# Kernel tuning notes

Hardware: AMD Instinct MI355X
Metric: run time of the kernel (lower is better)

## Reference

```python
import jax, jax.numpy as jnp
import numpy as np

B, N, D = 4, 512, 256  # batch, num_diseases, feature_dim == hidden_dim
H = 256                # hidden_dim
EPS = 1e-5

def _layernorm(x, g, b):
    m = jnp.mean(x, axis=-1, keepdims=True)
    v = jnp.mean((x - m) ** 2, axis=-1, keepdims=True)
    return (x - m) * jax.lax.rsqrt(v + EPS) * g + b

def setup_inputs() -> dict:
    key = jax.random.key(0)
    ks = jax.random.split(key, 16)
    s = 0.02
    return {
        "x": jax.random.normal(ks[0], (B, N, D), jnp.float32),
        "area_matrix": jax.random.uniform(ks[1], (B, N), jnp.float32),
        "co_occurrence": jax.random.uniform(ks[2], (N, N), jnp.float32),
        "Wq": jax.random.normal(ks[3], (H, D), jnp.float32) * s,
        "bq": jnp.zeros((H,), jnp.float32),
        "Wk": jax.random.normal(ks[4], (H, D), jnp.float32) * s,
        "bk": jnp.zeros((H,), jnp.float32),
        "Wv": jax.random.normal(ks[5], (H, D), jnp.float32) * s,
        "bv": jnp.zeros((H,), jnp.float32),
        "We1": jax.random.normal(ks[6], (H, 2), jnp.float32) * 0.5,
        "be1": jnp.zeros((H,), jnp.float32),
        "We2": jax.random.normal(ks[7], (1, H), jnp.float32) * s,
        "be2": jnp.zeros((1,), jnp.float32),
        "Wo": jax.random.normal(ks[8], (H, H), jnp.float32) * s,
        "bo": jnp.zeros((H,), jnp.float32),
        "g_ot": jnp.ones((H,), jnp.float32),
        "b_ot": jnp.zeros((H,), jnp.float32),
        "g1": jnp.ones((H,), jnp.float32),
        "b1": jnp.zeros((H,), jnp.float32),
        "g2": jnp.ones((H,), jnp.float32),
        "b2": jnp.zeros((H,), jnp.float32),
    }

def reference(x, area_matrix, co_occurrence, Wq, bq, Wk, bk, Wv, bv,
              We1, be1, We2, be2, Wo, bo, g_ot, b_ot, g1, b1, g2, b2):
    # projections: (B, N, H)
    q = jnp.einsum('bnd,hd->bnh', x, Wq) + bq
    k = jnp.einsum('bnd,hd->bnh', x, Wk) + bk
    v = jnp.einsum('bnd,hd->bnh', x, Wv) + bv
    attn_scores = jnp.einsum('bih,bjh->bij', q, k) / jnp.sqrt(jnp.float32(H))
    # edge inputs: (B, N, N, 2) = stack(broadcast area along last N, broadcast co-occ along batch)
    area = jnp.broadcast_to(area_matrix[:, :, None], (B, N, N))
    co = jnp.broadcast_to(co_occurrence[None], (B, N, N))
    edge_inputs = jnp.stack([area, co], axis=-1)
    h = jax.nn.relu(jnp.einsum('bije,he->bijh', edge_inputs, We1) + be1)
    edge_weights = jax.nn.sigmoid(jnp.einsum('bijh,oh->bijo', h, We2) + be2)[..., 0]
    attn_probs = jax.nn.softmax(attn_scores * edge_weights, axis=-1)  # dropout = identity (eval)
    out = jnp.einsum('bij,bjh->bih', attn_probs, v)
    out = _layernorm(out, g1, b1)
    out = jax.nn.relu(_layernorm(jnp.einsum('bnh,oh->bno', out, Wo) + bo, g_ot, b_ot))
    out = _layernorm(out + x, g2, b2)
    return out
```

## Files before the change

kernel.cpp:

```cpp
#include <hip/hip_runtime.h>

typedef unsigned short u16;
typedef unsigned int u32;

#define NB 4
#define NN 512
#define ND 256
#define NH 256
#define TI 4

typedef __attribute__((ext_vector_type(8))) short short8;
typedef __attribute__((ext_vector_type(4))) float f32x4;

__device__ __forceinline__ u16 bfq(float f) {
    u32 t; __builtin_memcpy(&t, &f, 4);
    u32 r = (t + 0x7FFFu + ((t >> 16) & 1u)) >> 16;
    return (u16)r;
}

__device__ __forceinline__ float waveReduceSum(float v) {
#pragma unroll
    for (int o = 32; o > 0; o >>= 1) v += __shfl_down(v, o);
    return v;
}

__device__ __forceinline__ void blockReduce8(float4& va, float4& vb, float4* red) {
#pragma unroll
    for (int o = 32; o > 0; o >>= 1) {
        va.x += __shfl_down(va.x, o); va.y += __shfl_down(va.y, o);
        va.z += __shfl_down(va.z, o); va.w += __shfl_down(va.w, o);
        vb.x += __shfl_down(vb.x, o); vb.y += __shfl_down(vb.y, o);
        vb.z += __shfl_down(vb.z, o); vb.w += __shfl_down(vb.w, o);
    }
    int wid = threadIdx.x >> 6;
    __syncthreads();
    if ((threadIdx.x & 63) == 0) { red[2 * wid] = va; red[2 * wid + 1] = vb; }
    __syncthreads();
    float4 ra = red[0], rb = red[1];
#pragma unroll
    for (int w = 1; w < 8; ++w) {
        float4 ua = red[2 * w], ub = red[2 * w + 1];
        ra.x += ua.x; ra.y += ua.y; ra.z += ua.z; ra.w += ua.w;
        rb.x += ub.x; rb.y += ub.y; rb.z += ub.z; rb.w += ub.w;
    }
    va = ra; vb = rb;
}

__global__ __launch_bounds__(256) void prep_kernel(
    const float* __restrict__ x, const float* __restrict__ Wq,
    const float* __restrict__ Wk, const float* __restrict__ Wv,
    const float* __restrict__ Wo,
    u16* __restrict__ xb, u16* __restrict__ wb)
{
    const int idx4 = (blockIdx.x * 256 + threadIdx.x) * 4;
    const float* src;
    u16* dst;
    int off;
    if (idx4 < 524288) { src = x; dst = xb; off = idx4; }
    else {
        int u = idx4 - 524288;
        int which = u >> 16; off = u & 65535;
        src = (which == 0) ? Wq : (which == 1) ? Wk : (which == 2) ? Wv : Wo;
        dst = wb + which * 65536;
    }
    float4 f = *(const float4*)(src + off);
    u32 lo = (u32)bfq(f.x) | ((u32)bfq(f.y) << 16);
    u32 hi = (u32)bfq(f.z) | ((u32)bfq(f.w) << 16);
    *(uint2*)(dst + off) = make_uint2(lo, hi);
}

__global__ __launch_bounds__(256) void qkv_mfma(
    const u16* __restrict__ xb, const u16* __restrict__ wb,
    const float* __restrict__ bq, const float* __restrict__ bk, const float* __restrict__ bv,
    u16* __restrict__ qb, u16* __restrict__ kb, u16* __restrict__ vt)
{
    const int lane = threadIdx.x & 63, wave = threadIdx.x >> 6;
    const int r0 = blockIdx.x * 64 + wave * 16;
    const int out0 = blockIdx.y * 16;
    const int which = blockIdx.y >> 4;
    const float* bia = (which == 0) ? bq : (which == 1) ? bk : bv;

    const int m = lane & 15, koff = (lane >> 4) * 8;
    const u16* Ap = xb + (size_t)(r0 + m) * 256 + koff;
    const u16* Bp = wb + which * 65536 + (size_t)((out0 & 255) + m) * 256 + koff;

    f32x4 acc = {0.f, 0.f, 0.f, 0.f};
#pragma unroll
    for (int ks = 0; ks < 8; ++ks) {
        short8 a  = *(const short8*)(Ap + ks * 32);
        short8 bb = *(const short8*)(Bp + ks * 32);
        acc = __builtin_amdgcn_mfma_f32_16x16x32_bf16(a, bb, acc, 0, 0, 0);
    }

    const int oc = (out0 + m) & 255;
    const float bias = bia[oc];
    const int rbase = r0 + (lane >> 4) * 4;
#pragma unroll
    for (int reg = 0; reg < 4; ++reg) {
        int R = rbase + reg;
        u16 val = bfq(acc[reg] + bias);
        if (which == 0)      qb[(size_t)R * 256 + oc] = val;
        else if (which == 1) kb[(size_t)R * 256 + oc] = val;
        else                 vt[((size_t)(R >> 9) * 256 + oc) * 512 + (R & 511)] = val;
    }
}

#define PSTR 520
#define YSTR 264
__global__ __launch_bounds__(512, 4) void fused_kernel(
    const float* __restrict__ x, const float* __restrict__ area, const float* __restrict__ co,
    const float* __restrict__ We1, const float* __restrict__ be1,
    const float* __restrict__ We2, const float* __restrict__ be2,
    const u16* __restrict__ wob, const float* __restrict__ bo,
    const float* __restrict__ g_ot, const float* __restrict__ b_ot,
    const float* __restrict__ g1, const float* __restrict__ b1,
    const float* __restrict__ g2, const float* __restrict__ b2,
    const u16* __restrict__ qb, const u16* __restrict__ kb,
    const u16* __restrict__ vt, float* __restrict__ out)
{
    const int tid = threadIdx.x;
    const int b = blockIdx.x >> 7;
    const int i0 = (blockIdx.x & 127) << 2;
    const int lane = tid & 63, w = tid >> 6;
    const int g = lane >> 4, c = lane & 15;
    const int hP = tid & 255, half = tid >> 8;

    __shared__ float histS[1024], histB[1024];
    __shared__ float pvbuf[1024];
    __shared__ u16 srow16[16 * PSTR];
    __shared__ u16 y16[16 * YSTR];
    __shared__ float4 red8b[16];
    __shared__ float sBaseS[4], sBaseB[4], redA[8], redB[8];

    const int m = lane & 15, koff = (lane >> 4) * 8;
    const u16* Ap    = qb + (size_t)(b * 512 + i0 + m) * 256 + koff;
    const u16* Kbase = kb + (size_t)(b * 512 + m) * 256 + koff;

    short8 afr[8];
#pragma unroll
    for (int ks = 0; ks < 8; ++ks) afr[ks] = *(const short8*)(Ap + ks * 32);
    short8 k0[4], k1[4];
#pragma unroll
    for (int ks = 0; ks < 4; ++ks)
        k0[ks] = *(const short8*)(Kbase + (size_t)(w * 4) * 16 * 256 + ks * 32);

    float cov[4];
#pragma unroll
    for (int t = 0; t < 4; ++t)
        cov[t] = co[(size_t)(i0 + g) * NN + (w * 4 + t) * 16 + c];

    float xv[TI];
#pragma unroll
    for (int ti = 0; ti < TI; ++ti)
        xv[ti] = x[(size_t)(b * NN + i0 + ti) * ND + hP];

    const float bov  = bo[hP];
    const float g1v  = g1[hP],  b1v  = b1[hP];
    const float gotv = g_ot[hP], botv = b_ot[hP];
    const float g2v  = g2[hP],  b2v  = b2[hP];
    const float be2f = be2[0];

    histS[tid] = 0.f; histS[tid + 512] = 0.f;
    histB[tid] = 0.f; histB[tid + 512] = 0.f;
    {
        u32* s32 = (u32*)srow16;
        for (int i = tid; i < 4160; i += 512) s32[i] = 0u;
        u32* y32 = (u32*)y16;
        for (int i = tid; i < 2112; i += 512) y32[i] = 0u;
    }
    __syncthreads();

    {
        const int s = tid >> 7, h0 = tid & 127;
        const float a = area[b * NN + i0 + s];
        float baS = 0.f, baB = 0.f;
#pragma unroll
        for (int k = 0; k < 2; ++k) {
            const int h = h0 + 128 * k;
            const float w10 = We1[2 * h], w11 = We1[2 * h + 1];
            const float w2v = We2[h], be1v = be1[h];
            const float al = fmaf(a, w10, be1v);
            const float sl = w11 * w2v, bb = al * w2v;
            if (w11 == 0.f) {
                if (al > 0.f) baB += bb;
            } else {
                float tt = -al / w11;
                if (w11 > 0.f) {
                    if (tt <= 0.f)      { baS += sl; baB += bb; }
                    else if (tt < 1.f) {
                        int u = (int)(tt * 256.f); u = u > 255 ? 255 : u;
                        atomicAdd(&histS[s * 256 + u], sl);
                        atomicAdd(&histB[s * 256 + u], bb);
                    }
                } else {
                    if (tt >= 1.f)      { baS += sl; baB += bb; }
                    else if (tt > 0.f) {
                        baS += sl; baB += bb;
                        int u = (int)(tt * 256.f); u = u > 255 ? 255 : u;
                        atomicAdd(&histS[s * 256 + u], -sl);
                        atomicAdd(&histB[s * 256 + u], -bb);
                    }
                }
            }
        }
        float rS = waveReduceSum(baS), rB = waveReduceSum(baB);
        if (lane == 0) { redA[w] = rS; redB[w] = rB; }
    }

    f32x4 sacc[4];
    {
#pragma unroll
        for (int t = 0; t < 4; ++t) {
            const u16* Bp = Kbase + (size_t)(w * 4 + t) * 16 * 256;
#pragma unroll
            for (int ks = 0; ks < 4; ++ks) k1[ks] = *(const short8*)(Bp + (ks + 4) * 32);
            f32x4 acc = {0.f, 0.f, 0.f, 0.f};
#pragma unroll
            for (int ks = 0; ks < 4; ++ks)
                acc = __builtin_amdgcn_mfma_f32_16x16x32_bf16(afr[ks], k0[ks], acc, 0, 0, 0);
            if (t < 3) {
                const u16* Bn = Kbase + (size_t)(w * 4 + t + 1) * 16 * 256;
#pragma unroll
                for (int ks = 0; ks < 4; ++ks) k0[ks] = *(const short8*)(Bn + ks * 32);
            }
#pragma unroll
            for (int ks = 0; ks < 4; ++ks)
                acc = __builtin_amdgcn_mfma_f32_16x16x32_bf16(afr[ks + 4], k1[ks], acc, 0, 0, 0);
            sacc[t] = acc;
        }
    }
    __syncthreads();
    if (tid < 4) {
        sBaseS[tid] = redA[2 * tid] + redA[2 * tid + 1];
        sBaseB[tid] = redB[2 * tid] + redB[2 * tid + 1];
    }

    {
        const int s = w & 3;
        float* hp = (w < 4) ? histS : histB;
        float b0 = hp[s * 256 + 4 * lane + 0];
        float b1 = hp[s * 256 + 4 * lane + 1];
        float b2 = hp[s * 256 + 4 * lane + 2];
        float b3 = hp[s * 256 + 4 * lane + 3];
        float p0 = b0, p1 = p0 + b1, p2 = p1 + b2, p3 = p2 + b3;
        float incl = p3;
#pragma unroll
        for (int off = 1; off < 64; off <<= 1) {
            float t = __shfl_up(incl, off);
            if (lane >= off) incl += t;
        }
        float excl = incl - p3;
        hp[s * 256 + 4 * lane + 0] = p0 + excl;
        hp[s * 256 + 4 * lane + 1] = p1 + excl;
        hp[s * 256 + 4 * lane + 2] = p2 + excl;
        hp[s * 256 + 4 * lane + 3] = p3 + excl;
    }
    __syncthreads();

    {
#pragma unroll
        for (int t = 0; t < 4; ++t) {
            const int j = (w * 4 + t) * 16 + c;
            float s0 = __shfl(sacc[t][0], c);
            float s1 = __shfl(sacc[t][1], c);
            float s2 = __shfl(sacc[t][2], c);
            float s3 = __shfl(sacc[t][3], c);
            float sv = (g == 0) ? s0 : (g == 1) ? s1 : (g == 2) ? s2 : s3;
            float cc = cov[t];
            int u = (int)(cc * 256.f); u = u > 255 ? 255 : u;
            float Sg = sBaseS[g] + histS[g * 256 + u];
            float Bg = sBaseB[g] + histB[g * 256 + u];
            float e = fmaf(cc, Sg, Bg) + be2f;
            float ew = 1.f / (1.f + __expf(-e));
            srow16[g * PSTR + j] = bfq(__expf(sv * 0.0625f * ew));
        }
    }
    __syncthreads();

    {
        const int t0 = 2 * w, t1 = 2 * w + 1;
        const u16* B0p = vt + ((size_t)(b * 256 + t0 * 16 + m)) * 512 + koff;
        const u16* B1p = vt + ((size_t)(b * 256 + t1 * 16 + m)) * 512 + koff;
        const u16* Arow = srow16 + m * PSTR + koff;
        f32x4 acc0 = {0.f, 0.f, 0.f, 0.f}, acc1 = {0.f, 0.f, 0.f, 0.f};
#pragma unroll
        for (int ks = 0; ks < 16; ++ks) {
            short8 a  = *(const short8*)(Arow + ks * 32);
            short8 b0 = *(const short8*)(B0p + ks * 32);
            short8 b1 = *(const short8*)(B1p + ks * 32);
            acc0 = __builtin_amdgcn_mfma_f32_16x16x32_bf16(a, b0, acc0, 0, 0, 0);
            acc1 = __builtin_amdgcn_mfma_f32_16x16x32_bf16(a, b1, acc1, 0, 0, 0);
        }
        if (lane < 16) {
#pragma unroll
            for (int reg = 0; reg < 4; ++reg) {
                pvbuf[reg * 256 + t0 * 16 + lane] = acc0[reg];
                pvbuf[reg * 256 + t1 * 16 + lane] = acc1[reg];
            }
        }
        __syncthreads();
    }

    float4 sa, sb;
    float accv[TI];
#pragma unroll
    for (int ti = 0; ti < TI; ++ti) {
        accv[ti] = (half == 0) ? pvbuf[ti * 256 + hP] : 0.f;
        ((float*)&sa)[ti] = accv[ti];
        ((float*)&sb)[ti] = accv[ti] * accv[ti];
    }
    blockReduce8(sa, sb, red8b);
    if (half == 0) {
#pragma unroll
        for (int ti = 0; ti < TI; ++ti) {
            float mean = ((const float*)&sa)[ti] * (1.f / 256.f);
            float var = fmaxf(((const float*)&sb)[ti] * (1.f / 256.f) - mean * mean, 0.f);
            y16[ti * YSTR + hP] = bfq((accv[ti] - mean) * rsqrtf(var + 1e-5f) * g1v + b1v);
        }
    }
    __syncthreads();

    {
        const int t0 = 2 * w, t1 = 2 * w + 1;
        const u16* B0p = wob + (size_t)(t0 * 16 + m) * 256 + koff;
        const u16* B1p = wob + (size_t)(t1 * 16 + m) * 256 + koff;
        const u16* Arow = y16 + m * YSTR + koff;
        f32x4 acc0 = {0.f, 0.f, 0.f, 0.f}, acc1 = {0.f, 0.f, 0.f, 0.f};
#pragma unroll
        for (int ks = 0; ks < 8; ++ks) {
            short8 a  = *(const short8*)(Arow + ks * 32);
            short8 b0 = *(const short8*)(B0p + ks * 32);
            short8 b1 = *(const short8*)(B1p + ks * 32);
            acc0 = __builtin_amdgcn_mfma_f32_16x16x32_bf16(a, b0, acc0, 0, 0, 0);
            acc1 = __builtin_amdgcn_mfma_f32_16x16x32_bf16(a, b1, acc1, 0, 0, 0);
        }
        if (lane < 16) {
#pragma unroll
            for (int reg = 0; reg < 4; ++reg) {
                pvbuf[reg * 256 + t0 * 16 + lane] = acc0[reg];
                pvbuf[reg * 256 + t1 * 16 + lane] = acc1[reg];
            }
        }
        __syncthreads();
    }

    float acc2[TI];
#pragma unroll
    for (int ti = 0; ti < TI; ++ti) {
        acc2[ti] = (half == 0) ? pvbuf[ti * 256 + hP] + bov : 0.f;
        ((float*)&sa)[ti] = acc2[ti];
        ((float*)&sb)[ti] = acc2[ti] * acc2[ti];
    }
    blockReduce8(sa, sb, red8b);
    float z[TI];
#pragma unroll
    for (int ti = 0; ti < TI; ++ti) {
        float mean = ((const float*)&sa)[ti] * (1.f / 256.f);
        float var = fmaxf(((const float*)&sb)[ti] * (1.f / 256.f) - mean * mean, 0.f);
        z[ti] = fmaxf((acc2[ti] - mean) * rsqrtf(var + 1e-5f) * gotv + botv, 0.f);
    }

    float tt[TI];
#pragma unroll
    for (int ti = 0; ti < TI; ++ti) {
        tt[ti] = (half == 0) ? z[ti] + xv[ti] : 0.f;
        ((float*)&sa)[ti] = tt[ti]; ((float*)&sb)[ti] = tt[ti] * tt[ti];
    }
    blockReduce8(sa, sb, red8b);
    if (half == 0) {
#pragma unroll
        for (int ti = 0; ti < TI; ++ti) {
            float mean = ((const float*)&sa)[ti] * (1.f / 256.f);
            float var = fmaxf(((const float*)&sb)[ti] * (1.f / 256.f) - mean * mean, 0.f);
            float o = (tt[ti] - mean) * rsqrtf(var + 1e-5f) * g2v + b2v;
            out[(size_t)(b * NN + i0 + ti) * NH + hP] = o;
        }
    }
}

extern "C" void kernel_launch(void* const* d_in, const int* in_sizes, int n_in,
                              void* d_out, int out_size, void* d_ws, size_t ws_size,
                              hipStream_t stream) {
    const float* x    = (const float*)d_in[0];
    const float* area = (const float*)d_in[1];
    const float* co   = (const float*)d_in[2];
    const float* Wq   = (const float*)d_in[3];
    const float* bq   = (const float*)d_in[4];
    const float* Wk   = (const float*)d_in[5];
    const float* bk   = (const float*)d_in[6];
    const float* Wv   = (const float*)d_in[7];
    const float* bv   = (const float*)d_in[8];
    const float* We1  = (const float*)d_in[9];
    const float* be1  = (const float*)d_in[10];
    const float* We2  = (const float*)d_in[11];
    const float* be2  = (const float*)d_in[12];
    const float* Wo   = (const float*)d_in[13];
    const float* bo   = (const float*)d_in[14];
    const float* g_ot = (const float*)d_in[15];
    const float* b_ot = (const float*)d_in[16];
    const float* g1   = (const float*)d_in[17];
    const float* b1   = (const float*)d_in[18];
    const float* g2   = (const float*)d_in[19];
    const float* b2   = (const float*)d_in[20];

    u16*  xb  = (u16*)d_ws;
    u16*  wb  = xb + (size_t)2048 * 256;
    u16*  qb  = wb + (size_t)4 * 65536;
    u16*  kb  = qb + (size_t)2048 * 256;
    u16*  vt  = kb + (size_t)2048 * 256;

    prep_kernel<<<768, 256, 0, stream>>>(x, Wq, Wk, Wv, Wo, xb, wb);
    qkv_mfma<<<dim3(32, 48), 256, 0, stream>>>(xb, wb, bq, bk, bv, qb, kb, vt);
    fused_kernel<<<NB * NN / TI, 512, 0, stream>>>(x, area, co, We1, be1, We2, be2,
                                                   wb + 3 * 65536, bo,
                                                   g_ot, b_ot, g1, b1, g2, b2,
                                                   qb, kb, vt, (float*)d_out);
}
```

Measured before the change: 161.3 us.

## Prefetch K/V/Wo into cache via dummy LDS loads and swizzle block order

Adds global_load_lds prefetches into a dummy LDS buffer at kernel start, so the K, V^T, Wo and co-occurrence rows (plus x and W in the QKV kernel) are pulled into cache early and their latency overlaps the histogram setup. It also remaps block indices so that consecutive blocks land on different XCD-style groups, and replaces the manual double-buffered K register loads with plain in-loop loads. This costs extra memory traffic and LDS write bandwidth, and every lane writes to the same dummy LDS location.

```diff
diff --git a/kernel.cpp b/kernel.cpp
--- a/kernel.cpp
+++ b/kernel.cpp
@@ -11,6 +11,12 @@
 
 typedef __attribute__((ext_vector_type(8))) short short8;
 typedef __attribute__((ext_vector_type(4))) float f32x4;
+
+typedef __attribute__((address_space(3))) u32 lds32_t;
+typedef __attribute__((address_space(1))) const u32 g32_t;
+__device__ __forceinline__ void pf16(const void* gp, u32* lp) {
+    __builtin_amdgcn_global_load_lds((g32_t*)gp, (lds32_t*)lp, 16, 0, 0);
+}
 
 __device__ __forceinline__ u16 bfq(float f) {
     u32 t; __builtin_memcpy(&t, &f, 4);
@@ -80,6 +86,17 @@
     const int which = blockIdx.y >> 4;
     const float* bia = (which == 0) ? bq : (which == 1) ? bk : bv;
 
+    __shared__ u32 pfdummy[256];
+
+    {
+        const u16* apre = xb + (size_t)(blockIdx.x * 64 + wave * 16) * 256;
+#pragma unroll
+        for (int q = 0; q < 8; ++q) pf16(apre + q * 512 + lane * 8, pfdummy);
+        const u16* bpre = wb + which * 65536 + (size_t)((out0 & 255) + wave * 4) * 256;
+#pragma unroll
+        for (int q = 0; q < 2; ++q) pf16(bpre + q * 512 + lane * 8, pfdummy);
+    }
+
     const int m = lane & 15, koff = (lane >> 4) * 8;
     const u16* Ap = xb + (size_t)(r0 + m) * 256 + koff;
     const u16* Bp = wb + which * 65536 + (size_t)((out0 & 255) + m) * 256 + koff;
@@ -119,8 +136,9 @@
     const u16* __restrict__ vt, float* __restrict__ out)
 {
     const int tid = threadIdx.x;
-    const int b = blockIdx.x >> 7;
-    const int i0 = (blockIdx.x & 127) << 2;
+    const int bsw = (blockIdx.x & 7) * 64 + (blockIdx.x >> 3);
+    const int b = bsw >> 7;
+    const int i0 = (bsw & 127) << 2;
     const int lane = tid & 63, w = tid >> 6;
     const int g = lane >> 4, c = lane & 15;
     const int hP = tid & 255, half = tid >> 8;
@@ -131,6 +149,7 @@
     __shared__ u16 y16[16 * YSTR];
     __shared__ float4 red8b[16];
     __shared__ float sBaseS[4], sBaseB[4], redA[8], redB[8];
+    __shared__ u32 pfdummy[256];
 
     const int m = lane & 15, koff = (lane >> 4) * 8;
     const u16* Ap    = qb + (size_t)(b * 512 + i0 + m) * 256 + koff;
@@ -139,10 +158,6 @@
     short8 afr[8];
 #pragma unroll
     for (int ks = 0; ks < 8; ++ks) afr[ks] = *(const short8*)(Ap + ks * 32);
-    short8 k0[4], k1[4];
-#pragma unroll
-    for (int ks = 0; ks < 4; ++ks)
-        k0[ks] = *(const short8*)(Kbase + (size_t)(w * 4) * 16 * 256 + ks * 32);
 
     float cov[4];
 #pragma unroll
@@ -159,6 +174,19 @@
     const float gotv = g_ot[hP], botv = b_ot[hP];
     const float g2v  = g2[hP],  b2v  = b2[hP];
     const float be2f = be2[0];
+
+    {
+        const u16* kpre = kb + (size_t)(b * 512 + w * 64) * 256;
+#pragma unroll
+        for (int q = 0; q < 32; ++q) pf16(kpre + q * 512 + lane * 8, pfdummy);
+        const u16* vpre = vt + (size_t)(b * 256 + w * 32) * 512;
+#pragma unroll
+        for (int q = 0; q < 32; ++q) pf16(vpre + q * 512 + lane * 8, pfdummy);
+        const u16* wpre = wob + (size_t)(w * 32) * 256;
+#pragma unroll
+        for (int q = 0; q < 16; ++q) pf16(wpre + q * 512 + lane * 8, pfdummy);
+        pf16(co + (size_t)(i0 + (w >> 1)) * 512 + (w & 1) * 256 + lane * 4, pfdummy);
+    }
 
     histS[tid] = 0.f; histS[tid + 512] = 0.f;
     histB[tid] = 0.f; histB[tid + 512] = 0.f;
@@ -212,20 +240,12 @@
 #pragma unroll
         for (int t = 0; t < 4; ++t) {
             const u16* Bp = Kbase + (size_t)(w * 4 + t) * 16 * 256;
-#pragma unroll
-            for (int ks = 0; ks < 4; ++ks) k1[ks] = *(const short8*)(Bp + (ks + 4) * 32);
             f32x4 acc = {0.f, 0.f, 0.f, 0.f};
 #pragma unroll
-            for (int ks = 0; ks < 4; ++ks)
-                acc = __builtin_amdgcn_mfma_f32_16x16x32_bf16(afr[ks], k0[ks], acc, 0, 0, 0);
-            if (t < 3) {
-                const u16* Bn = Kbase + (size_t)(w * 4 + t + 1) * 16 * 256;
-#pragma unroll
-                for (int ks = 0; ks < 4; ++ks) k0[ks] = *(const short8*)(Bn + ks * 32);
+            for (int ks = 0; ks < 8; ++ks) {
+                short8 bb = *(const short8*)(Bp + ks * 32);
+                acc = __builtin_amdgcn_mfma_f32_16x16x32_bf16(afr[ks], bb, acc, 0, 0, 0);
             }
-#pragma unroll
-            for (int ks = 0; ks < 4; ++ks)
-                acc = __builtin_amdgcn_mfma_f32_16x16x32_bf16(afr[ks + 4], k1[ks], acc, 0, 0, 0);
             sacc[t] = acc;
         }
     }
```

After: 172.5 us. 6.9% more time.

## Fold bf16 conversion into GEMM kernels, drop prep kernel, swizzle block order

Applied to the files above, without the earlier changes.

The separate prep kernel that converted x and the weights to bf16 is removed. qkv_mfma and the fused kernel now load fp32 directly and convert to bf16 in registers, which saves one launch and a round trip through the workspace. The fused kernel also remaps block indices with a swizzle and drops the manual K-fragment double-buffering in the score GEMM in favor of a simple loop. The trade-off is twice the global bytes per operand load, plus redundant conversion of Wo in every block of the fused kernel.

```diff
diff --git a/kernel.cpp b/kernel.cpp
--- a/kernel.cpp
+++ b/kernel.cpp
@@ -18,6 +18,15 @@
     return (u16)r;
 }
 
+__device__ __forceinline__ short8 cvt8(float4 a, float4 b) {
+    short8 r;
+    r[0] = (short)bfq(a.x); r[1] = (short)bfq(a.y);
+    r[2] = (short)bfq(a.z); r[3] = (short)bfq(a.w);
+    r[4] = (short)bfq(b.x); r[5] = (short)bfq(b.y);
+    r[6] = (short)bfq(b.z); r[7] = (short)bfq(b.w);
+    return r;
+}
+
 __device__ __forceinline__ float waveReduceSum(float v) {
 #pragma unroll
     for (int o = 32; o > 0; o >>= 1) v += __shfl_down(v, o);
@@ -46,50 +55,32 @@
     va = ra; vb = rb;
 }
 
-__global__ __launch_bounds__(256) void prep_kernel(
-    const float* __restrict__ x, const float* __restrict__ Wq,
-    const float* __restrict__ Wk, const float* __restrict__ Wv,
-    const float* __restrict__ Wo,
-    u16* __restrict__ xb, u16* __restrict__ wb)
-{
-    const int idx4 = (blockIdx.x * 256 + threadIdx.x) * 4;
-    const float* src;
-    u16* dst;
-    int off;
-    if (idx4 < 524288) { src = x; dst = xb; off = idx4; }
-    else {
-        int u = idx4 - 524288;
-        int which = u >> 16; off = u & 65535;
-        src = (which == 0) ? Wq : (which == 1) ? Wk : (which == 2) ? Wv : Wo;
-        dst = wb + which * 65536;
-    }
-    float4 f = *(const float4*)(src + off);
-    u32 lo = (u32)bfq(f.x) | ((u32)bfq(f.y) << 16);
-    u32 hi = (u32)bfq(f.z) | ((u32)bfq(f.w) << 16);
-    *(uint2*)(dst + off) = make_uint2(lo, hi);
-}
-
 __global__ __launch_bounds__(256) void qkv_mfma(
-    const u16* __restrict__ xb, const u16* __restrict__ wb,
-    const float* __restrict__ bq, const float* __restrict__ bk, const float* __restrict__ bv,
+    const float* __restrict__ x,
+    const float* __restrict__ Wq, const float* __restrict__ bq,
+    const float* __restrict__ Wk, const float* __restrict__ bk,
+    const float* __restrict__ Wv, const float* __restrict__ bv,
     u16* __restrict__ qb, u16* __restrict__ kb, u16* __restrict__ vt)
 {
     const int lane = threadIdx.x & 63, wave = threadIdx.x >> 6;
     const int r0 = blockIdx.x * 64 + wave * 16;
     const int out0 = blockIdx.y * 16;
     const int which = blockIdx.y >> 4;
+    const float* W   = (which == 0) ? Wq : (which == 1) ? Wk : Wv;
     const float* bia = (which == 0) ? bq : (which == 1) ? bk : bv;
 
     const int m = lane & 15, koff = (lane >> 4) * 8;
-    const u16* Ap = xb + (size_t)(r0 + m) * 256 + koff;
-    const u16* Bp = wb + which * 65536 + (size_t)((out0 & 255) + m) * 256 + koff;
+    const float* Apf = x + (size_t)(r0 + m) * 256 + koff;
+    const float* Bpf = W + (size_t)((out0 & 255) + m) * 256 + koff;
 
     f32x4 acc = {0.f, 0.f, 0.f, 0.f};
 #pragma unroll
     for (int ks = 0; ks < 8; ++ks) {
-        short8 a  = *(const short8*)(Ap + ks * 32);
-        short8 bb = *(const short8*)(Bp + ks * 32);
-        acc = __builtin_amdgcn_mfma_f32_16x16x32_bf16(a, bb, acc, 0, 0, 0);
+        float4 a0 = *(const float4*)(Apf + ks * 32);
+        float4 a1 = *(const float4*)(Apf + ks * 32 + 4);
+        float4 b0 = *(const float4*)(Bpf + ks * 32);
+        float4 b1 = *(const float4*)(Bpf + ks * 32 + 4);
+        acc = __builtin_amdgcn_mfma_f32_16x16x32_bf16(cvt8(a0, a1), cvt8(b0, b1), acc, 0, 0, 0);
     }
 
     const int oc = (out0 + m) & 255;
@@ -111,7 +102,7 @@
     const float* __restrict__ x, const float* __restrict__ area, const float* __restrict__ co,
     const float* __restrict__ We1, const float* __restrict__ be1,
     const float* __restrict__ We2, const float* __restrict__ be2,
-    const u16* __restrict__ wob, const float* __restrict__ bo,
+    const float* __restrict__ Wo, const float* __restrict__ bo,
     const float* __restrict__ g_ot, const float* __restrict__ b_ot,
     const float* __restrict__ g1, const float* __restrict__ b1,
     const float* __restrict__ g2, const float* __restrict__ b2,
@@ -119,8 +110,9 @@
     const u16* __restrict__ vt, float* __restrict__ out)
 {
     const int tid = threadIdx.x;
-    const int b = blockIdx.x >> 7;
-    const int i0 = (blockIdx.x & 127) << 2;
+    const int bsw = (blockIdx.x & 7) * 64 + (blockIdx.x >> 3);
+    const int b = bsw >> 7;
+    const int i0 = (bsw & 127) << 2;
     const int lane = tid & 63, w = tid >> 6;
     const int g = lane >> 4, c = lane & 15;
     const int hP = tid & 255, half = tid >> 8;
@@ -139,10 +131,6 @@
     short8 afr[8];
 #pragma unroll
     for (int ks = 0; ks < 8; ++ks) afr[ks] = *(const short8*)(Ap + ks * 32);
-    short8 k0[4], k1[4];
-#pragma unroll
-    for (int ks = 0; ks < 4; ++ks)
-        k0[ks] = *(const short8*)(Kbase + (size_t)(w * 4) * 16 * 256 + ks * 32);
 
     float cov[4];
 #pragma unroll
@@ -212,20 +200,12 @@
 #pragma unroll
         for (int t = 0; t < 4; ++t) {
             const u16* Bp = Kbase + (size_t)(w * 4 + t) * 16 * 256;
-#pragma unroll
-            for (int ks = 0; ks < 4; ++ks) k1[ks] = *(const short8*)(Bp + (ks + 4) * 32);
             f32x4 acc = {0.f, 0.f, 0.f, 0.f};
 #pragma unroll
-            for (int ks = 0; ks < 4; ++ks)
-                acc = __builtin_amdgcn_mfma_f32_16x16x32_bf16(afr[ks], k0[ks], acc, 0, 0, 0);
-            if (t < 3) {
-                const u16* Bn = Kbase + (size_t)(w * 4 + t + 1) * 16 * 256;
-#pragma unroll
-                for (int ks = 0; ks < 4; ++ks) k0[ks] = *(const short8*)(Bn + ks * 32);
+            for (int ks = 0; ks < 8; ++ks) {
+                short8 bb = *(const short8*)(Bp + ks * 32);
+                acc = __builtin_amdgcn_mfma_f32_16x16x32_bf16(afr[ks], bb, acc, 0, 0, 0);
             }
-#pragma unroll
-            for (int ks = 0; ks < 4; ++ks)
-                acc = __builtin_amdgcn_mfma_f32_16x16x32_bf16(afr[ks + 4], k1[ks], acc, 0, 0, 0);
             sacc[t] = acc;
         }
     }
@@ -322,15 +302,15 @@
 
     {
         const int t0 = 2 * w, t1 = 2 * w + 1;
-        const u16* B0p = wob + (size_t)(t0 * 16 + m) * 256 + koff;
-        const u16* B1p = wob + (size_t)(t1 * 16 + m) * 256 + koff;
+        const float* B0f = Wo + (size_t)(t0 * 16 + m) * 256 + koff;
+        const float* B1f = Wo + (size_t)(t1 * 16 + m) * 256 + koff;
         const u16* Arow = y16 + m * YSTR + koff;
         f32x4 acc0 = {0.f, 0.f, 0.f, 0.f}, acc1 = {0.f, 0.f, 0.f, 0.f};
 #pragma unroll
         for (int ks = 0; ks < 8; ++ks) {
             short8 a  = *(const short8*)(Arow + ks * 32);
-            short8 b0 = *(const short8*)(B0p + ks * 32);
-            short8 b1 = *(const short8*)(B1p + ks * 32);
+            short8 b0 = cvt8(*(const float4*)(B0f + ks * 32), *(const float4*)(B0f + ks * 32 + 4));
+            short8 b1 = cvt8(*(const float4*)(B1f + ks * 32), *(const float4*)(B1f + ks * 32 + 4));
             acc0 = __builtin_amdgcn_mfma_f32_16x16x32_bf16(a, b0, acc0, 0, 0, 0);
             acc1 = __builtin_amdgcn_mfma_f32_16x16x32_bf16(a, b1, acc1, 0, 0, 0);
         }
@@ -403,16 +383,12 @@
     const float* g2   = (const float*)d_in[19];
     const float* b2   = (const float*)d_in[20];
 
-    u16*  xb  = (u16*)d_ws;
-    u16*  wb  = xb + (size_t)2048 * 256;
-    u16*  qb  = wb + (size_t)4 * 65536;
+    u16*  qb  = (u16*)d_ws;
     u16*  kb  = qb + (size_t)2048 * 256;
     u16*  vt  = kb + (size_t)2048 * 256;
 
-    prep_kernel<<<768, 256, 0, stream>>>(x, Wq, Wk, Wv, Wo, xb, wb);
-    qkv_mfma<<<dim3(32, 48), 256, 0, stream>>>(xb, wb, bq, bk, bv, qb, kb, vt);
+    qkv_mfma<<<dim3(32, 48), 256, 0, stream>>>(x, Wq, bq, Wk, bk, Wv, bv, qb, kb, vt);
     fused_kernel<<<NB * NN / TI, 512, 0, stream>>>(x, area, co, We1, be1, We2, be2,
-                                                   wb + 3 * 65536, bo,
-                                                   g_ot, b_ot, g1, b1, g2, b2,
+                                                   Wo, bo, g_ot, b_ot, g1, b1, g2, b2,
                                                    qb, kb, vt, (float*)d_out);
 }
```

New measurement: 176.4 us. +9.4%, slower.
